# Optimization experiments

Hardware: AMD Instinct MI355X
Metric: run time of the kernel (lower is better)

The kernel has to match this reference:

```python
import jax, jax.numpy as jnp
import numpy as np

NUM_GROUPS = 8
EPS = 1e-5


def group_norm(x, scale, bias):
    # x: [b, c, h, w]; 8 groups, affine, eps=1e-5 (torch GroupNorm defaults)
    b, c, h, w = x.shape
    xg = x.reshape(b, NUM_GROUPS, c // NUM_GROUPS * h * w)
    mean = jnp.mean(xg, axis=-1, keepdims=True)
    var = jnp.var(xg, axis=-1, keepdims=True)
    xg = (xg - mean) * jax.lax.rsqrt(var + EPS)
    x = xg.reshape(b, c, h, w)
    return x * scale[None, :, None, None] + bias[None, :, None, None]


def conv1x1(x, w, bias):
    # 1x1 conv == per-pixel linear: x [b,c,h,w], w [c_out,c_in], bias [c_out]
    return jnp.einsum('oc,bchw->bohw', w, x) + bias[None, :, None, None]


def setup_inputs() -> dict:
    key = jax.random.key(0)
    ks = jax.random.split(key, 11)
    b, c, h, w = 8, 512, 32, 32
    init = 1.0 / np.sqrt(c)
    d = {
        'x': jax.random.normal(ks[0], (b, c, h, w), dtype=jnp.float32),
        'gn_scale': jnp.ones((c,), jnp.float32),
        'gn_bias': jnp.zeros((c,), jnp.float32),
        'wq': jax.random.uniform(ks[1], (c, c), jnp.float32, -init, init),
        'bq': jax.random.uniform(ks[2], (c,), jnp.float32, -init, init),
        'wk': jax.random.uniform(ks[3], (c, c), jnp.float32, -init, init),
        'bk': jax.random.uniform(ks[4], (c,), jnp.float32, -init, init),
        'wv': jax.random.uniform(ks[5], (c, c), jnp.float32, -init, init),
        'bv': jax.random.uniform(ks[6], (c,), jnp.float32, -init, init),
        'wproj': jax.random.uniform(ks[7], (c, c), jnp.float32, -init, init),
        'bproj': jax.random.uniform(ks[8], (c,), jnp.float32, -init, init),
    }
    return d


def reference(x, gn_scale, gn_bias, wq, bq, wk, bk, wv, bv, wproj, bproj):
    b, c, h, w = x.shape
    h_ = group_norm(x, gn_scale, gn_bias)
    q = conv1x1(h_, wq, bq).reshape(b, c, h * w)  # [b,c,hw]
    k = conv1x1(h_, wk, bk).reshape(b, c, h * w)
    v = conv1x1(h_, wv, bv).reshape(b, c, h * w)
    scale = 1.0 / np.sqrt(c).astype(np.float32)
    # scores[b,i,j] = sum_c q[b,c,i]*k[b,c,j]
    scores = jnp.einsum('bci,bcj->bij', q, k) * scale
    attn = jax.nn.softmax(scores, axis=2)  # softmax over j (keys)
    # h_[b,c,i] = sum_j v[b,c,j] * attn[b,i,j]
    out = jnp.einsum('bcj,bij->bci', v, attn).reshape(b, c, h, w)
    out = conv1x1(out, wproj, bproj)
    return x + out
```

## Files before the change

kernel.cpp:

```cpp
#include <hip/hip_runtime.h>
#include <hip/hip_bf16.h>
#include <hip/hip_cooperative_groups.h>

namespace cg = cooperative_groups;

#define DI __device__ __forceinline__

typedef __bf16 bf16x8 __attribute__((ext_vector_type(8)));
typedef float f32x4 __attribute__((ext_vector_type(4)));

typedef const void __attribute__((address_space(1))) gas_t;
typedef void __attribute__((address_space(3))) las_t;

DI unsigned short f2bf(float f) {
    unsigned u = __builtin_bit_cast(unsigned, f);
    u += 0x7fffu + ((u >> 16) & 1u);
    return (unsigned short)(u >> 16);
}

template <int ROWS>
DI void stage_tile(const unsigned short* __restrict__ g, int ldK,
                   unsigned short* lds, int t) {
    int row_in = t >> 3;
    int kg = (t & 7) ^ (row_in & 7);
    const unsigned short* src = g + (size_t)row_in * ldK + kg * 8;
    unsigned short* dst = lds + ((t >> 6) << 9);
#pragma unroll
    for (int c = 0; c < ROWS / 32; ++c) {
        __builtin_amdgcn_global_load_lds(
            (gas_t*)(unsigned long long)(src + (size_t)c * 32 * ldK),
            (las_t*)(unsigned)(unsigned long long)(dst + c * 2048),
            16, 0, 0);
    }
}

DI bf16x8 frag(const unsigned short* lds, int r, int kg) {
    return *(const bf16x8*)((const char*)lds + r * 128 + ((kg ^ (r & 7)) << 4));
}

template <int MR>
DI void compute_step(const unsigned short* As_, const unsigned short* Bs_,
                     f32x4 (&acc)[MR][4], int wm, int wn, int l15, int lks) {
#pragma unroll
    for (int kk = 0; kk < 2; ++kk) {
        bf16x8 a_[MR], b_[4];
#pragma unroll
        for (int m = 0; m < MR; ++m) a_[m] = frag(As_, wm + m * 16 + l15, kk * 4 + lks);
#pragma unroll
        for (int n = 0; n < 4; ++n) b_[n] = frag(Bs_, wn + n * 16 + l15, kk * 4 + lks);
#pragma unroll
        for (int m = 0; m < MR; ++m)
#pragma unroll
            for (int n = 0; n < 4; ++n)
                acc[m][n] = __builtin_amdgcn_mfma_f32_16x16x32_bf16(a_[m], b_[n], acc[m][n], 0, 0, 0);
    }
}

template <int TM, int MODE, int PIPE>
DI void gemm_phase(unsigned short* AsB, unsigned short* BsB,
                   const unsigned short* __restrict__ A, const unsigned short* __restrict__ B,
                   const float* __restrict__ b0, const float* __restrict__ b1,
                   const float* __restrict__ b2,
                   void* __restrict__ C0, void* __restrict__ C1, void* __restrict__ C2,
                   const float* __restrict__ resid, float* __restrict__ spart,
                   int M, int N, int K, float scale, size_t sA, size_t sB, size_t sC,
                   int bx, int t) {
    constexpr int MR = TM / 32;
    constexpr int ABUF = TM * 64;
    constexpr int BBUF = 128 * 64;
    int b = bx & 7;
    int tile = bx >> 3;
    int nTx = N >> 7;
    int tx = tile % nTx, ty = tile / nTx;
    int m0 = ty * TM, n0 = tx << 7;
    const unsigned short* Ag = A + sA * b + (size_t)m0 * K;
    const unsigned short* Bg = B + sB * b + (size_t)n0 * K;
    int lane = t & 63, wid = t >> 6;
    int wm = (wid >> 1) * (TM / 2), wn = (wid & 1) * 64;
    const int l15 = lane & 15, lks = lane >> 4;

    f32x4 acc[MR][4];
#pragma unroll
    for (int i = 0; i < MR; ++i)
#pragma unroll
        for (int j = 0; j < 4; ++j) acc[i][j] = (f32x4){0.f, 0.f, 0.f, 0.f};

    float inv[4];
    if constexpr (MODE == 2) {
#pragma unroll
        for (int n = 0; n < 4; ++n) {
            int ng = n0 + wn + n * 16 + l15;
            float ssum = 0.f;
#pragma unroll
            for (int k = 0; k < 16; ++k) ssum += spart[(size_t)(b * 16 + k) * 1024 + ng];
            inv[n] = 1.f / ssum;
        }
    }
    float bn4[4];
    if constexpr (MODE == 3) {
#pragma unroll
        for (int n = 0; n < 4; ++n) bn4[n] = b0[n0 + wn + n * 16 + l15];
    }

    if constexpr (PIPE == 0) {
        for (int k0 = 0; k0 < K; k0 += 64) {
            stage_tile<TM>(Ag + k0, K, AsB, t);
            stage_tile<128>(Bg + k0, K, BsB, t);
            asm volatile("s_waitcnt vmcnt(0)" ::: "memory");
            __syncthreads();
            compute_step<MR>(AsB, BsB, acc, wm, wn, l15, lks);
            __syncthreads();
        }
    } else {
        stage_tile<TM>(Ag, K, AsB, t);
        stage_tile<128>(Bg, K, BsB, t);
        asm volatile("s_waitcnt vmcnt(0)" ::: "memory");
        __syncthreads();
        int cur = 0;
        for (int k0 = 0; k0 < K; k0 += 64) {
            if (k0 + 64 < K) {
                stage_tile<TM>(Ag + k0 + 64, K, AsB + (cur ^ 1) * ABUF, t);
                stage_tile<128>(Bg + k0 + 64, K, BsB + (cur ^ 1) * BBUF, t);
            }
            compute_step<MR>(AsB + cur * ABUF, BsB + cur * BBUF, acc, wm, wn, l15, lks);
            if (k0 + 64 < K) {
                asm volatile("s_waitcnt vmcnt(0)" ::: "memory");
                __syncthreads();
            }
            cur ^= 1;
        }
    }

    const int rbase = lks * 4;
    const size_t cb = sC * b;
    if constexpr (MODE == 0) {
#pragma unroll
        for (int m = 0; m < MR; ++m) {
            int mgg = m0 + wm + m * 16 + rbase;
            int region = mgg >> 9;
            int local = mgg & 511;
            const float* bias = (region == 0) ? b0 : (region == 1) ? b1 : b2;
            float bv4[4];
#pragma unroll
            for (int j = 0; j < 4; ++j) bv4[j] = bias[local + j];
            if (region < 2) {
                unsigned short* Ct = (unsigned short*)(region == 0 ? C0 : C1) + cb;
#pragma unroll
                for (int n = 0; n < 4; ++n) {
                    int ng = n0 + wn + n * 16 + l15;
                    f32x4 v = acc[m][n];
                    ushort4 o;
                    o.x = f2bf(v[0] + bv4[0]); o.y = f2bf(v[1] + bv4[1]);
                    o.z = f2bf(v[2] + bv4[2]); o.w = f2bf(v[3] + bv4[3]);
                    *(ushort4*)&Ct[(size_t)ng * 512 + local] = o;
                }
            } else {
                unsigned short* Vb = (unsigned short*)C2 + cb;
#pragma unroll
                for (int n = 0; n < 4; ++n) {
                    int ng = n0 + wn + n * 16 + l15;
                    f32x4 v = acc[m][n];
#pragma unroll
                    for (int j = 0; j < 4; ++j)
                        Vb[(size_t)(local + j) * 1024 + ng] = f2bf(v[j] + bv4[j]);
                }
            }
        }
    } else if constexpr (MODE == 1) {
        unsigned short* Ct = (unsigned short*)C0 + cb;
        float psum[4] = {0.f, 0.f, 0.f, 0.f};
#pragma unroll
        for (int m = 0; m < MR; ++m) {
            int mg = m0 + wm + m * 16 + rbase;
#pragma unroll
            for (int n = 0; n < 4; ++n) {
                int ng = n0 + wn + n * 16 + l15;
                f32x4 v = acc[m][n];
                float e0 = __expf(v[0] * scale), e1 = __expf(v[1] * scale);
                float e2 = __expf(v[2] * scale), e3 = __expf(v[3] * scale);
                psum[n] += (e0 + e1) + (e2 + e3);
                ushort4 o;
                o.x = f2bf(e0); o.y = f2bf(e1); o.z = f2bf(e2); o.w = f2bf(e3);
                *(ushort4*)&Ct[(size_t)ng * M + mg] = o;
            }
        }
        int rb = (m0 >> 7) * 2 + (wid >> 1);
#pragma unroll
        for (int n = 0; n < 4; ++n) {
            float p = psum[n];
            p += __shfl_xor(p, 16);
            p += __shfl_xor(p, 32);
            if (lks == 0) {
                int ng = n0 + wn + n * 16 + l15;
                spart[(size_t)(b * 16 + rb) * 1024 + ng] = p;
            }
        }
    } else if constexpr (MODE == 2) {
        unsigned short* Ct = (unsigned short*)C0 + cb;
#pragma unroll
        for (int m = 0; m < MR; ++m) {
            int mg = m0 + wm + m * 16 + rbase;
#pragma unroll
            for (int n = 0; n < 4; ++n) {
                int ng = n0 + wn + n * 16 + l15;
                f32x4 v = acc[m][n];
                ushort4 o;
                o.x = f2bf(v[0] * inv[n]); o.y = f2bf(v[1] * inv[n]);
                o.z = f2bf(v[2] * inv[n]); o.w = f2bf(v[3] * inv[n]);
                *(ushort4*)&Ct[(size_t)ng * M + mg] = o;
            }
        }
    } else {
        float* Cf = (float*)C0 + cb;
#pragma unroll
        for (int m = 0; m < MR; ++m) {
            int mg = m0 + wm + m * 16 + rbase;
#pragma unroll
            for (int n = 0; n < 4; ++n) {
                int ng = n0 + wn + n * 16 + l15;
                f32x4 v = acc[m][n];
                const float* rp = resid + cb + (size_t)ng * M + mg;
                float4 o;
                o.x = v[0] + bn4[n] + rp[0]; o.y = v[1] + bn4[n] + rp[1];
                o.z = v[2] + bn4[n] + rp[2]; o.w = v[3] + bn4[n] + rp[3];
                *(float4*)&Cf[(size_t)ng * M + mg] = o;
            }
        }
    }
}

DI void stats_wcvt_body(const float* __restrict__ x, float2* __restrict__ part,
                        const float* __restrict__ w0, const float* __restrict__ w1,
                        const float* __restrict__ w2, const float* __restrict__ w3,
                        unsigned short* __restrict__ wb, float* red,
                        int bx, int t, int nchunk) {
    int b = bx & 7, g = (bx >> 3) & 7, ch = bx >> 6;
    size_t base = ((size_t)b * 512 + g * 64 + ch * 8) * 1024;
    const float4* xp = (const float4*)(x + base);
    float s = 0.f, q = 0.f;
#pragma unroll
    for (int it = 0; it < 8; ++it) {
        float4 v = xp[it * 256 + t];
        s += (v.x + v.y) + (v.z + v.w);
        q += (v.x * v.x + v.y * v.y) + (v.z * v.z + v.w * v.w);
    }
#pragma unroll
    for (int o = 32; o; o >>= 1) { s += __shfl_xor(s, o); q += __shfl_xor(q, o); }
    int lane = t & 63, wid = t >> 6;
    if (!lane) { red[wid] = s; red[4 + wid] = q; }
    __syncthreads();
    if (t == 0)
        part[((b * 8 + g) * 8) + ch] =
            make_float2(red[0] + red[1] + red[2] + red[3],
                        red[4] + red[5] + red[6] + red[7]);
    for (int cc = 0; cc < nchunk; ++cc) {
        int chunk = bx * nchunk + cc;
        int w = chunk >> 8;
        const float* sp = (w == 0) ? w0 : (w == 1) ? w1 : (w == 2) ? w2 : w3;
        unsigned short* o = wb + (size_t)w * 262144;
        int idx = (chunk & 255) * 256 + t;
        float4 v = ((const float4*)sp)[idx];
        ushort4 r;
        r.x = f2bf(v.x); r.y = f2bf(v.y); r.z = f2bf(v.z); r.w = f2bf(v.w);
        ((ushort4*)o)[idx] = r;
    }
}

DI void gn_apply_body(const float* __restrict__ x, const float2* __restrict__ part,
                      const float* __restrict__ gs, const float* __restrict__ gb,
                      unsigned short* __restrict__ hT, unsigned short* tile,
                      int bx, int t) {
    int b = bx & 7, g = (bx >> 3) & 7, ic = bx >> 6;
    int bg = b * 8 + g;
    float s = 0.f, q = 0.f;
#pragma unroll
    for (int k = 0; k < 8; ++k) { float2 p = part[bg * 8 + k]; s += p.x; q += p.y; }
    float mean = s * (1.f / 65536.f);
    float var = q * (1.f / 65536.f) - mean * mean;
    float rstd = rsqrtf(var + 1e-5f);

    int i4 = t & 31, cq = t >> 5;
    size_t xbase = ((size_t)b * 512 + g * 64) * 1024 + ic * 128;
#pragma unroll
    for (int pass = 0; pass < 8; ++pass) {
        int c = pass * 8 + cq;
        float4 v = *(const float4*)&x[xbase + (size_t)c * 1024 + i4 * 4];
        int gc = g * 64 + c;
        float sc = gs[gc] * rstd, bi = gb[gc] - mean * sc;
        unsigned short* tp = &tile[(i4 * 4) * 66 + c];
        tp[0]   = f2bf(v.x * sc + bi);
        tp[66]  = f2bf(v.y * sc + bi);
        tp[132] = f2bf(v.z * sc + bi);
        tp[198] = f2bf(v.w * sc + bi);
    }
    __syncthreads();
    int i = t >> 1, h = t & 1;
    const unsigned short* tp2 = &tile[i * 66 + h * 32];
    unsigned short* op = &hT[(size_t)b * (1024 * 512) + (size_t)(ic * 128 + i) * 512 + g * 64 + h * 32];
#pragma unroll
    for (int cc = 0; cc < 4; ++cc) {
        unsigned short tmp[8];
#pragma unroll
        for (int j = 0; j < 8; ++j) tmp[j] = tp2[cc * 8 + j];
        *(uint4*)&op[cc * 8] = *(const uint4*)tmp;
    }
}

struct Params {
    const float *x, *gs, *gb, *wq, *bq, *wk, *bk, *wv, *bv, *wp, *bp;
    float* out;
    unsigned short *hT, *wb, *qT, *kT, *vN, *E, *OT;
    float2* gnpart;
    float* spart;
};

__global__ __launch_bounds__(256, 2) void fused_kernel(Params p) {
    __shared__ __align__(16) unsigned short smem[32768];
    cg::grid_group grid = cg::this_grid();
    int bx = blockIdx.x, t = threadIdx.x;
    const size_t sH = 1024 * 512;
    const size_t sS = 1024 * 1024;

    stats_wcvt_body(p.x, p.gnpart, p.wq, p.wk, p.wv, p.wp, p.wb, (float*)smem, bx, t, 2);
    grid.sync();
    gn_apply_body(p.x, p.gnpart, p.gs, p.gb, p.hT, smem, bx, t);
    grid.sync();
    gemm_phase<192, 0, 0>(smem, smem + 12288, p.wb, p.hT, p.bq, p.bk, p.bv,
                          p.qT, p.kT, p.vN, nullptr, nullptr,
                          1536, 1024, 512, 1.f, 0, sH, sH, bx, t);
    grid.sync();
    gemm_phase<128, 1, 1>(smem, smem + 16384, p.kT, p.qT, nullptr, nullptr, nullptr,
                          p.E, nullptr, nullptr, nullptr, p.spart,
                          1024, 1024, 512, 0.044194173824159216f, sH, sH, sS, bx, t);
    grid.sync();
    gemm_phase<64, 2, 1>(smem, smem + 8192, p.vN, p.E, nullptr, nullptr, nullptr,
                         p.OT, nullptr, nullptr, nullptr, p.spart,
                         512, 1024, 1024, 1.f, sH, sS, sH, bx, t);
    grid.sync();
    gemm_phase<64, 3, 1>(smem, smem + 8192, p.OT, p.wb + 3 * 262144, p.bp, nullptr, nullptr,
                         p.out, nullptr, nullptr, p.x, nullptr,
                         1024, 512, 512, 1.f, sH, 0, sH, bx, t);
}

__global__ __launch_bounds__(256) void prep_kernel(const float* __restrict__ x,
                                                   float2* __restrict__ part,
                                                   const float* __restrict__ w0,
                                                   const float* __restrict__ w1,
                                                   const float* __restrict__ w2,
                                                   const float* __restrict__ w3,
                                                   unsigned short* __restrict__ wb) {
    __shared__ float red[8];
    int bx = blockIdx.x, t = threadIdx.x;
    if (bx < 512) {
        stats_wcvt_body(x, part, w0, w1, w2, w3, wb, red, bx, t, 0);
    } else {
        int chunk = bx - 512;
        int w = chunk >> 8;
        const float* sp = (w == 0) ? w0 : (w == 1) ? w1 : (w == 2) ? w2 : w3;
        unsigned short* o = wb + (size_t)w * 262144;
        int idx = (chunk & 255) * 256 + t;
        float4 v = ((const float4*)sp)[idx];
        ushort4 r;
        r.x = f2bf(v.x); r.y = f2bf(v.y); r.z = f2bf(v.z); r.w = f2bf(v.w);
        ((ushort4*)o)[idx] = r;
    }
}

__global__ __launch_bounds__(256) void gn_applyT(const float* __restrict__ x,
                                                 const float2* __restrict__ part,
                                                 const float* __restrict__ gs,
                                                 const float* __restrict__ gb,
                                                 unsigned short* __restrict__ hT) {
    __shared__ unsigned short tile[128 * 66];
    gn_apply_body(x, part, gs, gb, hT, tile, blockIdx.x, threadIdx.x);
}

template <int TM, int MODE, int MINW, int PIPE>
__global__ __launch_bounds__(256, MINW) void gemm_bt(
        const unsigned short* __restrict__ A, const unsigned short* __restrict__ B,
        const float* __restrict__ b0, const float* __restrict__ b1,
        const float* __restrict__ b2,
        void* __restrict__ C0, void* __restrict__ C1, void* __restrict__ C2,
        const float* __restrict__ resid, float* __restrict__ spart,
        int M, int N, int K, float scale, size_t sA, size_t sB, size_t sC) {
    constexpr int NBUF = PIPE ? 2 : 1;
    __shared__ __align__(16) unsigned short As[NBUF * TM * 64];
    __shared__ __align__(16) unsigned short Bs[NBUF * 128 * 64];
    gemm_phase<TM, MODE, PIPE>(As, Bs, A, B, b0, b1, b2, C0, C1, C2, resid, spart,
                               M, N, K, scale, sA, sB, sC, blockIdx.x, threadIdx.x);
}

extern "C" void kernel_launch(void* const* d_in, const int* in_sizes, int n_in,
                              void* d_out, int out_size, void* d_ws, size_t ws_size,
                              hipStream_t stream) {
    const float* x  = (const float*)d_in[0];
    const float* gs = (const float*)d_in[1];
    const float* gb = (const float*)d_in[2];
    const float* wq = (const float*)d_in[3];
    const float* bq = (const float*)d_in[4];
    const float* wk = (const float*)d_in[5];
    const float* bk = (const float*)d_in[6];
    const float* wv = (const float*)d_in[7];
    const float* bv = (const float*)d_in[8];
    const float* wp = (const float*)d_in[9];
    const float* bp = (const float*)d_in[10];
    float* out = (float*)d_out;

    char* ws = (char*)d_ws;
    const size_t MB = 1u << 20;
    unsigned short* hT = (unsigned short*)(ws + 0);
    unsigned short* wb = (unsigned short*)(ws + 8 * MB);
    unsigned short* qT = (unsigned short*)(ws + 10 * MB);
    unsigned short* kT = (unsigned short*)(ws + 18 * MB);
    unsigned short* vN = (unsigned short*)(ws + 26 * MB);
    unsigned short* E  = (unsigned short*)(ws + 34 * MB);
    unsigned short* OT = (unsigned short*)(ws + 50 * MB);
    float2* gnpart     = (float2*)(ws + 58 * MB);
    float*  spart      = (float*)(ws + 58 * MB + 65536);

    const unsigned short* wpb = wb + 3 * 262144;
    const size_t sH = 1024 * 512;
    const size_t sS = 1024 * 1024;

    int dev = 0;
    (void)hipGetDevice(&dev);
    int coop = 0;
    (void)hipDeviceGetAttribute(&coop, hipDeviceAttributeCooperativeLaunch, dev);
    int maxB = 0;
    (void)hipOccupancyMaxActiveBlocksPerMultiprocessor(&maxB, fused_kernel, 256, 0);
    if (coop && maxB >= 2) {
        Params p;
        p.x = x; p.gs = gs; p.gb = gb; p.wq = wq; p.bq = bq; p.wk = wk; p.bk = bk;
        p.wv = wv; p.bv = bv; p.wp = wp; p.bp = bp; p.out = out;
        p.hT = hT; p.wb = wb; p.qT = qT; p.kT = kT; p.vN = vN; p.E = E; p.OT = OT;
        p.gnpart = gnpart; p.spart = spart;
        void* args[] = {&p};
        hipError_t rc = hipLaunchCooperativeKernel(fused_kernel, dim3(512), dim3(256),
                                                   args, 0u, stream);
        if (rc == hipSuccess) return;
        (void)hipGetLastError();
    }

    prep_kernel<<<1536, 256, 0, stream>>>(x, gnpart, wq, wk, wv, wp, wb);
    gn_applyT<<<512, 256, 0, stream>>>(x, gnpart, gs, gb, hT);
    gemm_bt<128, 0, 3, 0><<<96 * 8, 256, 0, stream>>>(
        wb, hT, bq, bk, bv, qT, kT, vN, nullptr, nullptr,
        1536, 1024, 512, 1.f, 0, sH, sH);
    gemm_bt<128, 1, 2, 1><<<64 * 8, 256, 0, stream>>>(
        kT, qT, nullptr, nullptr, nullptr, E, nullptr, nullptr, nullptr, spart,
        1024, 1024, 512, 0.044194173824159216f, sH, sH, sS);
    gemm_bt<64, 2, 2, 1><<<64 * 8, 256, 0, stream>>>(
        vN, E, nullptr, nullptr, nullptr, OT, nullptr, nullptr, nullptr, spart,
        512, 1024, 1024, 1.f, sH, sS, sH);
    gemm_bt<64, 3, 2, 1><<<64 * 8, 256, 0, stream>>>(
        OT, wpb, bp, nullptr, nullptr, out, nullptr, nullptr, x, nullptr,
        1024, 512, 512, 1.f, sH, 0, sH);
}
```

Before: 75.87 us.

## Drop cooperative fused kernel; defer softmax normalization to projection GEMM and retile

Removes the cooperative single-kernel path with grid syncs, so the separate-kernel sequence always runs. Softmax row normalization moves out of the attn·V GEMM epilogue into the output-projection epilogue, and the attn·V GEMM swaps its operands (E as A, 128-row tiles, 256 blocks) to write OT with scalar stores. The QKV GEMM now uses a 192-row tile with double buffering. This removes grid-wide sync overhead but adds launch gaps, and the strided scalar bf16 stores in mode 2 may be poorly coalesced.

```diff
diff --git a/kernel.cpp b/kernel.cpp
--- a/kernel.cpp
+++ b/kernel.cpp
@@ -1,8 +1,5 @@
 #include <hip/hip_runtime.h>
 #include <hip/hip_bf16.h>
-#include <hip/hip_cooperative_groups.h>
-
-namespace cg = cooperative_groups;
 
 #define DI __device__ __forceinline__
 
@@ -78,6 +75,7 @@
     int lane = t & 63, wid = t >> 6;
     int wm = (wid >> 1) * (TM / 2), wn = (wid & 1) * 64;
     const int l15 = lane & 15, lks = lane >> 4;
+    const int rbase = lks * 4;
 
     f32x4 acc[MR][4];
 #pragma unroll
@@ -85,21 +83,23 @@
 #pragma unroll
         for (int j = 0; j < 4; ++j) acc[i][j] = (f32x4){0.f, 0.f, 0.f, 0.f};
 
-    float inv[4];
-    if constexpr (MODE == 2) {
-#pragma unroll
-        for (int n = 0; n < 4; ++n) {
-            int ng = n0 + wn + n * 16 + l15;
-            float ssum = 0.f;
-#pragma unroll
-            for (int k = 0; k < 16; ++k) ssum += spart[(size_t)(b * 16 + k) * 1024 + ng];
-            inv[n] = 1.f / ssum;
-        }
-    }
     float bn4[4];
+    float invm[MR][4];
     if constexpr (MODE == 3) {
 #pragma unroll
         for (int n = 0; n < 4; ++n) bn4[n] = b0[n0 + wn + n * 16 + l15];
+#pragma unroll
+        for (int m = 0; m < MR; ++m) {
+            int mrow = m0 + wm + m * 16 + rbase;
+#pragma unroll
+            for (int j = 0; j < 4; ++j) {
+                float ss = 0.f;
+#pragma unroll
+                for (int k = 0; k < 16; ++k)
+                    ss += spart[(size_t)(b * 16 + k) * 1024 + mrow + j];
+                invm[m][j] = 1.f / ss;
+            }
+        }
     }
 
     if constexpr (PIPE == 0) {
@@ -131,7 +131,6 @@
         }
     }
 
-    const int rbase = lks * 4;
     const size_t cb = sC * b;
     if constexpr (MODE == 0) {
 #pragma unroll
@@ -196,7 +195,7 @@
             }
         }
     } else if constexpr (MODE == 2) {
-        unsigned short* Ct = (unsigned short*)C0 + cb;
+        unsigned short* Ob = (unsigned short*)C0 + cb;
 #pragma unroll
         for (int m = 0; m < MR; ++m) {
             int mg = m0 + wm + m * 16 + rbase;
@@ -204,10 +203,9 @@
             for (int n = 0; n < 4; ++n) {
                 int ng = n0 + wn + n * 16 + l15;
                 f32x4 v = acc[m][n];
-                ushort4 o;
-                o.x = f2bf(v[0] * inv[n]); o.y = f2bf(v[1] * inv[n]);
-                o.z = f2bf(v[2] * inv[n]); o.w = f2bf(v[3] * inv[n]);
-                *(ushort4*)&Ct[(size_t)ng * M + mg] = o;
+#pragma unroll
+                for (int j = 0; j < 4; ++j)
+                    Ob[(size_t)(mg + j) * N + ng] = f2bf(v[j]);
             }
         }
     } else {
@@ -221,19 +219,18 @@
                 f32x4 v = acc[m][n];
                 const float* rp = resid + cb + (size_t)ng * M + mg;
                 float4 o;
-                o.x = v[0] + bn4[n] + rp[0]; o.y = v[1] + bn4[n] + rp[1];
-                o.z = v[2] + bn4[n] + rp[2]; o.w = v[3] + bn4[n] + rp[3];
+                o.x = v[0] * invm[m][0] + bn4[n] + rp[0];
+                o.y = v[1] * invm[m][1] + bn4[n] + rp[1];
+                o.z = v[2] * invm[m][2] + bn4[n] + rp[2];
+                o.w = v[3] * invm[m][3] + bn4[n] + rp[3];
                 *(float4*)&Cf[(size_t)ng * M + mg] = o;
             }
         }
     }
 }
 
-DI void stats_wcvt_body(const float* __restrict__ x, float2* __restrict__ part,
-                        const float* __restrict__ w0, const float* __restrict__ w1,
-                        const float* __restrict__ w2, const float* __restrict__ w3,
-                        unsigned short* __restrict__ wb, float* red,
-                        int bx, int t, int nchunk) {
+DI void stats_body(const float* __restrict__ x, float2* __restrict__ part,
+                   float* red, int bx, int t) {
     int b = bx & 7, g = (bx >> 3) & 7, ch = bx >> 6;
     size_t base = ((size_t)b * 512 + g * 64 + ch * 8) * 1024;
     const float4* xp = (const float4*)(x + base);
@@ -253,8 +250,21 @@
         part[((b * 8 + g) * 8) + ch] =
             make_float2(red[0] + red[1] + red[2] + red[3],
                         red[4] + red[5] + red[6] + red[7]);
-    for (int cc = 0; cc < nchunk; ++cc) {
-        int chunk = bx * nchunk + cc;
+}
+
+__global__ __launch_bounds__(256) void prep_kernel(const float* __restrict__ x,
+                                                   float2* __restrict__ part,
+                                                   const float* __restrict__ w0,
+                                                   const float* __restrict__ w1,
+                                                   const float* __restrict__ w2,
+                                                   const float* __restrict__ w3,
+                                                   unsigned short* __restrict__ wb) {
+    __shared__ float red[8];
+    int bx = blockIdx.x, t = threadIdx.x;
+    if (bx < 512) {
+        stats_body(x, part, red, bx, t);
+    } else {
+        int chunk = bx - 512;
         int w = chunk >> 8;
         const float* sp = (w == 0) ? w0 : (w == 1) ? w1 : (w == 2) ? w2 : w3;
         unsigned short* o = wb + (size_t)w * 262144;
@@ -266,10 +276,13 @@
     }
 }
 
-DI void gn_apply_body(const float* __restrict__ x, const float2* __restrict__ part,
-                      const float* __restrict__ gs, const float* __restrict__ gb,
-                      unsigned short* __restrict__ hT, unsigned short* tile,
-                      int bx, int t) {
+__global__ __launch_bounds__(256) void gn_applyT(const float* __restrict__ x,
+                                                 const float2* __restrict__ part,
+                                                 const float* __restrict__ gs,
+                                                 const float* __restrict__ gb,
+                                                 unsigned short* __restrict__ hT) {
+    __shared__ unsigned short tile[128 * 66];
+    int bx = blockIdx.x, t = threadIdx.x;
     int b = bx & 7, g = (bx >> 3) & 7, ic = bx >> 6;
     int bg = b * 8 + g;
     float s = 0.f, q = 0.f;
@@ -304,75 +317,6 @@
         for (int j = 0; j < 8; ++j) tmp[j] = tp2[cc * 8 + j];
         *(uint4*)&op[cc * 8] = *(const uint4*)tmp;
     }
-}
-
-struct Params {
-    const float *x, *gs, *gb, *wq, *bq, *wk, *bk, *wv, *bv, *wp, *bp;
-    float* out;
-    unsigned short *hT, *wb, *qT, *kT, *vN, *E, *OT;
-    float2* gnpart;
-    float* spart;
-};
-
-__global__ __launch_bounds__(256, 2) void fused_kernel(Params p) {
-    __shared__ __align__(16) unsigned short smem[32768];
-    cg::grid_group grid = cg::this_grid();
-    int bx = blockIdx.x, t = threadIdx.x;
-    const size_t sH = 1024 * 512;
-    const size_t sS = 1024 * 1024;
-
-    stats_wcvt_body(p.x, p.gnpart, p.wq, p.wk, p.wv, p.wp, p.wb, (float*)smem, bx, t, 2);
-    grid.sync();
-    gn_apply_body(p.x, p.gnpart, p.gs, p.gb, p.hT, smem, bx, t);
-    grid.sync();
-    gemm_phase<192, 0, 0>(smem, smem + 12288, p.wb, p.hT, p.bq, p.bk, p.bv,
-                          p.qT, p.kT, p.vN, nullptr, nullptr,
-                          1536, 1024, 512, 1.f, 0, sH, sH, bx, t);
-    grid.sync();
-    gemm_phase<128, 1, 1>(smem, smem + 16384, p.kT, p.qT, nullptr, nullptr, nullptr,
-                          p.E, nullptr, nullptr, nullptr, p.spart,
-                          1024, 1024, 512, 0.044194173824159216f, sH, sH, sS, bx, t);
-    grid.sync();
-    gemm_phase<64, 2, 1>(smem, smem + 8192, p.vN, p.E, nullptr, nullptr, nullptr,
-                         p.OT, nullptr, nullptr, nullptr, p.spart,
-                         512, 1024, 1024, 1.f, sH, sS, sH, bx, t);
-    grid.sync();
-    gemm_phase<64, 3, 1>(smem, smem + 8192, p.OT, p.wb + 3 * 262144, p.bp, nullptr, nullptr,
-                         p.out, nullptr, nullptr, p.x, nullptr,
-                         1024, 512, 512, 1.f, sH, 0, sH, bx, t);
-}
-
-__global__ __launch_bounds__(256) void prep_kernel(const float* __restrict__ x,
-                                                   float2* __restrict__ part,
-                                                   const float* __restrict__ w0,
-                                                   const float* __restrict__ w1,
-                                                   const float* __restrict__ w2,
-                                                   const float* __restrict__ w3,
-                                                   unsigned short* __restrict__ wb) {
-    __shared__ float red[8];
-    int bx = blockIdx.x, t = threadIdx.x;
-    if (bx < 512) {
-        stats_wcvt_body(x, part, w0, w1, w2, w3, wb, red, bx, t, 0);
-    } else {
-        int chunk = bx - 512;
-        int w = chunk >> 8;
-        const float* sp = (w == 0) ? w0 : (w == 1) ? w1 : (w == 2) ? w2 : w3;
-        unsigned short* o = wb + (size_t)w * 262144;
-        int idx = (chunk & 255) * 256 + t;
-        float4 v = ((const float4*)sp)[idx];
-        ushort4 r;
-        r.x = f2bf(v.x); r.y = f2bf(v.y); r.z = f2bf(v.z); r.w = f2bf(v.w);
-        ((ushort4*)o)[idx] = r;
-    }
-}
-
-__global__ __launch_bounds__(256) void gn_applyT(const float* __restrict__ x,
-                                                 const float2* __restrict__ part,
-                                                 const float* __restrict__ gs,
-                                                 const float* __restrict__ gb,
-                                                 unsigned short* __restrict__ hT) {
-    __shared__ unsigned short tile[128 * 66];
-    gn_apply_body(x, part, gs, gb, hT, tile, blockIdx.x, threadIdx.x);
 }
 
 template <int TM, int MODE, int MINW, int PIPE>
@@ -422,37 +366,19 @@
     const size_t sH = 1024 * 512;
     const size_t sS = 1024 * 1024;
 
-    int dev = 0;
-    (void)hipGetDevice(&dev);
-    int coop = 0;
-    (void)hipDeviceGetAttribute(&coop, hipDeviceAttributeCooperativeLaunch, dev);
-    int maxB = 0;
-    (void)hipOccupancyMaxActiveBlocksPerMultiprocessor(&maxB, fused_kernel, 256, 0);
-    if (coop && maxB >= 2) {
-        Params p;
-        p.x = x; p.gs = gs; p.gb = gb; p.wq = wq; p.bq = bq; p.wk = wk; p.bk = bk;
-        p.wv = wv; p.bv = bv; p.wp = wp; p.bp = bp; p.out = out;
-        p.hT = hT; p.wb = wb; p.qT = qT; p.kT = kT; p.vN = vN; p.E = E; p.OT = OT;
-        p.gnpart = gnpart; p.spart = spart;
-        void* args[] = {&p};
-        hipError_t rc = hipLaunchCooperativeKernel(fused_kernel, dim3(512), dim3(256),
-                                                   args, 0u, stream);
-        if (rc == hipSuccess) return;
-        (void)hipGetLastError();
-    }
-
     prep_kernel<<<1536, 256, 0, stream>>>(x, gnpart, wq, wk, wv, wp, wb);
     gn_applyT<<<512, 256, 0, stream>>>(x, gnpart, gs, gb, hT);
-    gemm_bt<128, 0, 3, 0><<<96 * 8, 256, 0, stream>>>(
+
+    gemm_bt<192, 0, 2, 1><<<512, 256, 0, stream>>>(
         wb, hT, bq, bk, bv, qT, kT, vN, nullptr, nullptr,
         1536, 1024, 512, 1.f, 0, sH, sH);
-    gemm_bt<128, 1, 2, 1><<<64 * 8, 256, 0, stream>>>(
+    gemm_bt<128, 1, 2, 1><<<512, 256, 0, stream>>>(
         kT, qT, nullptr, nullptr, nullptr, E, nullptr, nullptr, nullptr, spart,
         1024, 1024, 512, 0.044194173824159216f, sH, sH, sS);
-    gemm_bt<64, 2, 2, 1><<<64 * 8, 256, 0, stream>>>(
-        vN, E, nullptr, nullptr, nullptr, OT, nullptr, nullptr, nullptr, spart,
-        512, 1024, 1024, 1.f, sH, sS, sH);
-    gemm_bt<64, 3, 2, 1><<<64 * 8, 256, 0, stream>>>(
-        OT, wpb, bp, nullptr, nullptr, out, nullptr, nullptr, x, nullptr,
+    gemm_bt<128, 2, 2, 1><<<256, 256, 0, stream>>>(
+        E, vN, nullptr, nullptr, nullptr, OT, nullptr, nullptr, nullptr, nullptr,
+        1024, 512, 1024, 1.f, sS, sH, sH);
+    gemm_bt<64, 3, 2, 1><<<512, 256, 0, stream>>>(
+        OT, wpb, bp, nullptr, nullptr, out, nullptr, nullptr, x, spart,
         1024, 512, 512, 1.f, sH, 0, sH);
 }
```

Result: slower. 78.28 us (+3.2%).
